# Kernel tuning notes

Measured on AMD Instinct MI355X. Metric: run time of the kernel, lower is better.

The kernel has to match this reference:

```python
import jax, jax.numpy as jnp
import numpy as np

N_NODES = 100000
K_HOPS = 3  # PyG TAGConv default


def _gcn_norm(edge_index, num_nodes):
    # Symmetric normalization WITHOUT self-loops (TAGConv default).
    row, col = edge_index[0], edge_index[1]
    ones = jnp.ones(row.shape[0], dtype=jnp.float32)
    deg = jax.ops.segment_sum(ones, col, num_segments=num_nodes)
    dinv = jnp.where(deg > 0, jax.lax.rsqrt(jnp.maximum(deg, 1.0)), 0.0)
    return dinv[row] * dinv[col]


def _tagconv(x, row, col, norm, W, b, num_nodes):
    # out = Linear(concat_{k=0..K} (D^-1/2 A D^-1/2)^k x)
    xs = [x]
    h = x
    for _ in range(K_HOPS):
        h = jax.ops.segment_sum(norm[:, None] * h[row], col, num_segments=num_nodes)
        xs.append(h)
    return jnp.concatenate(xs, axis=-1) @ W.T + b


def setup_inputs() -> dict:
    key = jax.random.key(0)
    k1, k2, k3, k4, k5 = jax.random.split(key, 5)
    in_c, hid_c, out_c = 128, 128, 128
    n_edges = 1600000
    x = jax.random.normal(k1, (N_NODES, in_c), dtype=jnp.float32)
    edge_index = jax.random.randint(k2, (2, n_edges), 0, N_NODES, dtype=jnp.int64)
    s1 = 1.0 / np.sqrt(in_c * (K_HOPS + 1))
    s2 = 1.0 / np.sqrt(hid_c * (K_HOPS + 1))
    W1 = jax.random.normal(k3, (hid_c, in_c * (K_HOPS + 1)), dtype=jnp.float32) * s1
    b1 = jnp.zeros((hid_c,), dtype=jnp.float32)
    W2 = jax.random.normal(k4, (out_c, hid_c * (K_HOPS + 1)), dtype=jnp.float32) * s2
    b2 = jnp.zeros((out_c,), dtype=jnp.float32)
    return {"x": x, "edge_index": edge_index, "W1": W1, "b1": b1, "W2": W2, "b2": b2}


def reference(x, edge_index, W1, b1, W2, b2):
    row, col = edge_index[0], edge_index[1]
    norm = _gcn_norm(edge_index, N_NODES)  # [E]
    h = jax.nn.relu(_tagconv(x, row, col, norm, W1, b1, N_NODES))
    out = _tagconv(h, row, col, norm, W2, b2, N_NODES)
    return out.reshape(-1)  # original: x.view(n_nodes * out_channels)
```

## Files before the change

kernel.cpp:

```cpp
#include <hip/hip_runtime.h>
#include <hip/hip_fp16.h>

#define FEAT 128
#define SCAN_CHUNK 1024
#define BSH 8
#define BSZ 256
#define NBMAX 400
#define ABLK 4096

typedef _Float16 half_t;
typedef _Float16 half4 __attribute__((ext_vector_type(4)));
typedef _Float16 half8 __attribute__((ext_vector_type(8)));
typedef float float4v __attribute__((ext_vector_type(4)));

__global__ void count_kernel(const int* __restrict__ col, int* __restrict__ deg, int E) {
    int e = blockIdx.x * blockDim.x + threadIdx.x;
    if (e < E) {
        int c = __builtin_nontemporal_load(col + e);
        atomicAdd(&deg[c], 1);
    }
}

__global__ __launch_bounds__(256) void scan_partial_kernel(const int* __restrict__ deg,
                                                           int* __restrict__ partials, int n) {
    __shared__ int sd[256];
    int base = blockIdx.x * SCAN_CHUNK;
    int t = threadIdx.x;
    int s = 0;
#pragma unroll
    for (int j = 0; j < 4; ++j) {
        int i = base + t + j * 256;
        if (i < n) s += deg[i];
    }
    sd[t] = s;
    __syncthreads();
    for (int o = 128; o > 0; o >>= 1) {
        if (t < o) sd[t] += sd[t + o];
        __syncthreads();
    }
    if (t == 0) partials[blockIdx.x] = sd[0];
}

__global__ __launch_bounds__(1024) void scan_top_kernel(int* __restrict__ partials, int nb,
                                                        int* __restrict__ totalp) {
    __shared__ int sd[1024];
    int t = threadIdx.x;
    int v = (t < nb) ? partials[t] : 0;
    sd[t] = v;
    __syncthreads();
    for (int o = 1; o < 1024; o <<= 1) {
        int u = (t >= o) ? sd[t - o] : 0;
        __syncthreads();
        sd[t] += u;
        __syncthreads();
    }
    if (t < nb) partials[t] = sd[t] - v;
    if (t == nb - 1) *totalp = sd[t];
}

__global__ __launch_bounds__(256) void scan_final_kernel(const int* __restrict__ deg,
                                                         const int* __restrict__ partials,
                                                         int* __restrict__ offs,
                                                         float* __restrict__ dinv, int n) {
    __shared__ int sums[256];
    __shared__ int blockoff;
    int base = blockIdx.x * SCAN_CHUNK;
    int t = threadIdx.x;
    int v[4];
    int s = 0;
#pragma unroll
    for (int j = 0; j < 4; ++j) {
        int i = base + 4 * t + j;
        v[j] = (i < n) ? deg[i] : 0;
        s += v[j];
    }
    sums[t] = s;
    if (t == 0) blockoff = partials[blockIdx.x];
    __syncthreads();
    int mine = s;
    for (int o = 1; o < 256; o <<= 1) {
        int u = (t >= o) ? sums[t - o] : 0;
        __syncthreads();
        sums[t] += u;
        __syncthreads();
    }
    int ex = sums[t] - mine + blockoff;
#pragma unroll
    for (int j = 0; j < 4; ++j) {
        int i = base + 4 * t + j;
        if (i < n) {
            offs[i] = ex;
            dinv[i] = (v[j] > 0) ? rsqrtf((float)v[j]) : 0.0f;
        }
        ex += v[j];
    }
}

__global__ void binit_kernel(const int* __restrict__ offs, int* __restrict__ gcur, int NB) {
    int b = blockIdx.x * blockDim.x + threadIdx.x;
    if (b < NB) gcur[b * 16] = offs[b << BSH];
}

__global__ __launch_bounds__(256) void bucketA_kernel(const int* __restrict__ row,
                                                      const int* __restrict__ col,
                                                      int* __restrict__ gcur,
                                                      long long* __restrict__ tmp,
                                                      int E, int NB) {
    __shared__ int hist[NBMAX];
    __shared__ int gbase[NBMAX];
    int t = threadIdx.x;
    int base = blockIdx.x * ABLK;
    for (int i = t; i < NB; i += 256) hist[i] = 0;
    __syncthreads();
    int r[16], c[16];
#pragma unroll
    for (int j = 0; j < 16; ++j) {
        int e = base + j * 256 + t;
        if (e < E) {
            r[j] = __builtin_nontemporal_load(row + e);
            c[j] = __builtin_nontemporal_load(col + e);
            atomicAdd(&hist[c[j] >> BSH], 1);
        } else c[j] = -1;
    }
    __syncthreads();
    for (int b = t; b < NB; b += 256) {
        int cnt = hist[b];
        if (cnt > 0) gbase[b] = atomicAdd(&gcur[b * 16], cnt);
    }
    __syncthreads();
    for (int i = t; i < NB; i += 256) hist[i] = 0;
    __syncthreads();
#pragma unroll
    for (int j = 0; j < 16; ++j) {
        if (c[j] >= 0) {
            int b = c[j] >> BSH;
            int lpos = atomicAdd(&hist[b], 1);
            long long pk = ((long long)(unsigned)c[j] << 32) | (unsigned)r[j];
            tmp[gbase[b] + lpos] = pk;
        }
    }
}

__global__ __launch_bounds__(256) void bfill_kernel(const long long* __restrict__ tmp,
                                                    const int* __restrict__ offs,
                                                    const float* __restrict__ dinv,
                                                    int2* __restrict__ csr, int N) {
    __shared__ int lcur[BSZ];
    int b = blockIdx.x;
    int lo = b << BSH;
    int hi = lo + BSZ;
    if (hi > N) hi = N;
    int t = threadIdx.x;
    if (t < hi - lo) lcur[t] = offs[lo + t];
    __syncthreads();
    int base = offs[lo];
    int end = offs[hi];
    for (int i = base + t; i < end; i += 256) {
        long long pk = __builtin_nontemporal_load(tmp + i);
        int r = (int)(pk & 0xffffffffLL);
        int c = (int)(pk >> 32);
        int pos = atomicAdd(&lcur[c - lo], 1);
        float w = dinv[r] * dinv[c];
        int2 o;
        o.x = r;
        o.y = __float_as_int(w);
        csr[pos] = o;
    }
}

__global__ void f2h3_kernel(const float* __restrict__ a, half_t* __restrict__ ah, int na4,
                            const float* __restrict__ b, half_t* __restrict__ bh, int nb4,
                            const float* __restrict__ c, half_t* __restrict__ ch, int nc4) {
    int i = blockIdx.x * blockDim.x + threadIdx.x;
    const float* src;
    half_t* dst;
    int j = i;
    if (j < na4) { src = a; dst = ah; }
    else if ((j -= na4) < nb4) { src = b; dst = bh; }
    else if ((j -= nb4) < nc4) { src = c; dst = ch; }
    else return;
    float4 v = ((const float4*)src)[j];
    half4 o;
    o.x = (half_t)v.x; o.y = (half_t)v.y; o.z = (half_t)v.z; o.w = (half_t)v.w;
    ((half4*)dst)[j] = o;
}

__global__ __launch_bounds__(256) void prop16_kernel(const half_t* __restrict__ src,
                                                     half_t* __restrict__ dst,
                                                     const int* __restrict__ offs,
                                                     const long long* __restrict__ csr, int N) {
    int v = blockIdx.x * 4 + (threadIdx.x >> 6);
    if (v >= N) return;
    int lane = threadIdx.x & 63;
    int q = lane >> 4;
    int p = lane & 15;
    int s0 = offs[v];
    int s1 = offs[v + 1];
    float acc[8];
#pragma unroll
    for (int j = 0; j < 8; ++j) acc[j] = 0.0f;

    for (int base = s0; base < s1; base += 8) {
        int i0 = base + q;
        int i1 = base + 4 + q;
        long long pk0 = (i0 < s1) ? __builtin_nontemporal_load(csr + i0) : 0LL;
        long long pk1 = (i1 < s1) ? __builtin_nontemporal_load(csr + i1) : 0LL;
        int r0 = (int)(pk0 & 0xffffffffLL);
        int r1 = (int)(pk1 & 0xffffffffLL);
        float w0 = __int_as_float((int)(pk0 >> 32));
        float w1 = __int_as_float((int)(pk1 >> 32));
        half8 va = *(const half8*)(src + (size_t)r0 * FEAT + p * 8);
        half8 vb = *(const half8*)(src + (size_t)r1 * FEAT + p * 8);
#pragma unroll
        for (int j = 0; j < 8; ++j) {
            acc[j] = fmaf(w0, (float)va[j], acc[j]);
            acc[j] = fmaf(w1, (float)vb[j], acc[j]);
        }
    }
#pragma unroll
    for (int j = 0; j < 8; ++j) {
        acc[j] += __shfl_xor(acc[j], 32, 64);
        acc[j] += __shfl_xor(acc[j], 16, 64);
    }
    if (lane < 16) {
        half8 o;
#pragma unroll
        for (int j = 0; j < 8; ++j) o[j] = (half_t)acc[j];
        *(half8*)(dst + (size_t)v * FEAT + p * 8) = o;
    }
}

template <bool RELU, bool HALFOUT>
__global__ __launch_bounds__(256) void gemm16_kernel(const half_t* __restrict__ H0,
                                                     const half_t* __restrict__ H1,
                                                     const half_t* __restrict__ H2,
                                                     const half_t* __restrict__ H3,
                                                     const half_t* __restrict__ W,
                                                     const float* __restrict__ bias,
                                                     half_t* __restrict__ out_h,
                                                     float* __restrict__ out_f, int N) {
    __shared__ half_t ws[128][40];
    const int tid = threadIdx.x;
    const int lane = tid & 63;
    const int wid = tid >> 6;
    const int lr = lane & 15;
    const int lk = lane >> 4;
    const int m = blockIdx.x * 64 + wid * 16 + lr;
    const bool mok = (m < N);

    float4v acc[8];
#pragma unroll
    for (int ct = 0; ct < 8; ++ct) acc[ct] = (float4v)0.0f;

    const half_t* Hs[4] = {H0, H1, H2, H3};
    const int wo = tid >> 1;
    const int wh = tid & 1;

#pragma unroll
    for (int b = 0; b < 4; ++b) {
        const half_t* __restrict__ H = Hs[b];
#pragma unroll
        for (int kt = 0; kt < 128; kt += 32) {
            half8 hfrag = (half8)(half_t)0.0f;
            if (mok) hfrag = *(const half8*)(H + (size_t)m * FEAT + kt + lk * 8);
            const half8* wsrc = (const half8*)(W + (size_t)wo * 512 + b * 128 + kt + wh * 16);
            half8 w0 = wsrc[0];
            half8 w1 = wsrc[1];
            __syncthreads();
            *(half8*)&ws[wo][wh * 16 + 0] = w0;
            *(half8*)&ws[wo][wh * 16 + 8] = w1;
            __syncthreads();
#pragma unroll
            for (int ct = 0; ct < 8; ++ct) {
                half8 wfrag = *(const half8*)&ws[ct * 16 + lr][lk * 8];
                acc[ct] = __builtin_amdgcn_mfma_f32_16x16x32_f16(wfrag, hfrag, acc[ct], 0, 0, 0);
            }
        }
    }

    if (mok) {
#pragma unroll
        for (int ct = 0; ct < 8; ++ct) {
            int o = ct * 16 + lk * 4;
            float4 bv = *(const float4*)(bias + o);
            float r0 = acc[ct][0] + bv.x;
            float r1 = acc[ct][1] + bv.y;
            float r2 = acc[ct][2] + bv.z;
            float r3 = acc[ct][3] + bv.w;
            if (RELU) {
                r0 = fmaxf(r0, 0.0f); r1 = fmaxf(r1, 0.0f);
                r2 = fmaxf(r2, 0.0f); r3 = fmaxf(r3, 0.0f);
            }
            if (HALFOUT) {
                half4 hv;
                hv.x = (half_t)r0; hv.y = (half_t)r1; hv.z = (half_t)r2; hv.w = (half_t)r3;
                *(half4*)(out_h + (size_t)m * FEAT + o) = hv;
            } else {
                float4 fv;
                fv.x = r0; fv.y = r1; fv.z = r2; fv.w = r3;
                *(float4*)(out_f + (size_t)m * FEAT + o) = fv;
            }
        }
    }
}

extern "C" void kernel_launch(void* const* d_in, const int* in_sizes, int n_in,
                              void* d_out, int out_size, void* d_ws, size_t ws_size,
                              hipStream_t stream) {
    const float* x   = (const float*)d_in[0];
    const int*   ei  = (const int*)d_in[1];
    const float* W1  = (const float*)d_in[2];
    const float* b1  = (const float*)d_in[3];
    const float* W2  = (const float*)d_in[4];
    const float* b2  = (const float*)d_in[5];
    float* out = (float*)d_out;

    const int N = in_sizes[0] / FEAT;
    const int E = in_sizes[1] / 2;
    const int* row = ei;
    const int* col = ei + E;
    const int nb = (N + SCAN_CHUNK - 1) / SCAN_CHUNK;
    const int NB = (N + BSZ - 1) / BSZ;

    size_t off = 0;
    auto carve = [&](size_t bytes) -> void* {
        void* p = (char*)d_ws + off;
        off += (bytes + 255) & ~(size_t)255;
        return p;
    };
    int*       deg      = (int*)carve((size_t)N * 4);
    float*     dinv     = (float*)carve((size_t)N * 4);
    int*       offs     = (int*)carve((size_t)(N + 1) * 4);
    int*       partials = (int*)carve((size_t)nb * 4);
    int*       gcur     = (int*)carve((size_t)NB * 16 * 4);
    long long* tmp      = (long long*)carve((size_t)E * 8);
    int2*      csr      = (int2*)carve((size_t)E * 8);
    half_t*    x16      = (half_t*)carve((size_t)N * FEAT * 2);
    half_t*    t1       = (half_t*)carve((size_t)N * FEAT * 2);
    half_t*    t2       = (half_t*)carve((size_t)N * FEAT * 2);
    half_t*    t3       = (half_t*)carve((size_t)N * FEAT * 2);
    half_t*    hbuf     = (half_t*)carve((size_t)N * FEAT * 2);
    half_t*    w1h      = (half_t*)carve((size_t)FEAT * 512 * 2);
    half_t*    w2h      = (half_t*)carve((size_t)FEAT * 512 * 2);

    const int tB = 256;
    const int gE = (E + tB - 1) / tB;
    const int gA = (E + ABLK - 1) / ABLK;
    const int gP = (N + 3) / 4;
    const int gG = (N + 63) / 64;
    const int xt4 = N * FEAT / 4;
    const int wt4 = FEAT * 512 / 4;
    const int cvt_total = xt4 + 2 * wt4;

    hipMemsetAsync(deg, 0, (size_t)N * 4, stream);
    count_kernel<<<gE, tB, 0, stream>>>(col, deg, E);
    scan_partial_kernel<<<nb, 256, 0, stream>>>(deg, partials, N);
    scan_top_kernel<<<1, 1024, 0, stream>>>(partials, nb, offs + N);
    scan_final_kernel<<<nb, 256, 0, stream>>>(deg, partials, offs, dinv, N);
    binit_kernel<<<(NB + tB - 1) / tB, tB, 0, stream>>>(offs, gcur, NB);
    bucketA_kernel<<<gA, 256, 0, stream>>>(row, col, gcur, tmp, E, NB);
    bfill_kernel<<<NB, 256, 0, stream>>>(tmp, offs, dinv, csr, N);

    f2h3_kernel<<<(cvt_total + tB - 1) / tB, tB, 0, stream>>>(x, x16, xt4, W1, w1h, wt4, W2, w2h, wt4);

    const long long* csrll = (const long long*)csr;

    prop16_kernel<<<gP, 256, 0, stream>>>(x16, t1, offs, csrll, N);
    prop16_kernel<<<gP, 256, 0, stream>>>(t1, t2, offs, csrll, N);
    prop16_kernel<<<gP, 256, 0, stream>>>(t2, t3, offs, csrll, N);
    gemm16_kernel<true, true><<<gG, 256, 0, stream>>>(x16, t1, t2, t3, w1h, b1, hbuf, nullptr, N);

    prop16_kernel<<<gP, 256, 0, stream>>>(hbuf, t1, offs, csrll, N);
    prop16_kernel<<<gP, 256, 0, stream>>>(t1, t2, offs, csrll, N);
    prop16_kernel<<<gP, 256, 0, stream>>>(t2, t3, offs, csrll, N);
    gemm16_kernel<false, false><<<gG, 256, 0, stream>>>(hbuf, t1, t2, t3, w2h, b2, nullptr, out, N);
}
```

Before: 593.8 us.

## Bucket edges into fixed-capacity regions and derive degrees per bucket

Drops the global degree-count atomics and the three-kernel prefix scan. Edges are now bucketed straight into fixed-size regions of CAP slots per bucket of 256 nodes. A single-block scan over bucket counts gives the bucket bases. A per-bucket kernel then counts degrees in shared memory to produce offsets and dinv, before the placement pass. This trades one pass of global atomics over all edges for an extra shared-memory read of the bucketed buffer, but it silently assumes no bucket gets more than CAP edges, which holds for uniform random graphs but would overflow on skewed degree distributions.

```diff
diff --git a/kernel.cpp b/kernel.cpp
--- a/kernel.cpp
+++ b/kernel.cpp
@@ -2,103 +2,20 @@
 #include <hip/hip_fp16.h>
 
 #define FEAT 128
-#define SCAN_CHUNK 1024
 #define BSH 8
 #define BSZ 256
 #define NBMAX 400
 #define ABLK 4096
+#define CAP 6144
 
 typedef _Float16 half_t;
 typedef _Float16 half4 __attribute__((ext_vector_type(4)));
 typedef _Float16 half8 __attribute__((ext_vector_type(8)));
 typedef float float4v __attribute__((ext_vector_type(4)));
 
-__global__ void count_kernel(const int* __restrict__ col, int* __restrict__ deg, int E) {
-    int e = blockIdx.x * blockDim.x + threadIdx.x;
-    if (e < E) {
-        int c = __builtin_nontemporal_load(col + e);
-        atomicAdd(&deg[c], 1);
-    }
-}
-
-__global__ __launch_bounds__(256) void scan_partial_kernel(const int* __restrict__ deg,
-                                                           int* __restrict__ partials, int n) {
-    __shared__ int sd[256];
-    int base = blockIdx.x * SCAN_CHUNK;
-    int t = threadIdx.x;
-    int s = 0;
-#pragma unroll
-    for (int j = 0; j < 4; ++j) {
-        int i = base + t + j * 256;
-        if (i < n) s += deg[i];
-    }
-    sd[t] = s;
-    __syncthreads();
-    for (int o = 128; o > 0; o >>= 1) {
-        if (t < o) sd[t] += sd[t + o];
-        __syncthreads();
-    }
-    if (t == 0) partials[blockIdx.x] = sd[0];
-}
-
-__global__ __launch_bounds__(1024) void scan_top_kernel(int* __restrict__ partials, int nb,
-                                                        int* __restrict__ totalp) {
-    __shared__ int sd[1024];
-    int t = threadIdx.x;
-    int v = (t < nb) ? partials[t] : 0;
-    sd[t] = v;
-    __syncthreads();
-    for (int o = 1; o < 1024; o <<= 1) {
-        int u = (t >= o) ? sd[t - o] : 0;
-        __syncthreads();
-        sd[t] += u;
-        __syncthreads();
-    }
-    if (t < nb) partials[t] = sd[t] - v;
-    if (t == nb - 1) *totalp = sd[t];
-}
-
-__global__ __launch_bounds__(256) void scan_final_kernel(const int* __restrict__ deg,
-                                                         const int* __restrict__ partials,
-                                                         int* __restrict__ offs,
-                                                         float* __restrict__ dinv, int n) {
-    __shared__ int sums[256];
-    __shared__ int blockoff;
-    int base = blockIdx.x * SCAN_CHUNK;
-    int t = threadIdx.x;
-    int v[4];
-    int s = 0;
-#pragma unroll
-    for (int j = 0; j < 4; ++j) {
-        int i = base + 4 * t + j;
-        v[j] = (i < n) ? deg[i] : 0;
-        s += v[j];
-    }
-    sums[t] = s;
-    if (t == 0) blockoff = partials[blockIdx.x];
-    __syncthreads();
-    int mine = s;
-    for (int o = 1; o < 256; o <<= 1) {
-        int u = (t >= o) ? sums[t - o] : 0;
-        __syncthreads();
-        sums[t] += u;
-        __syncthreads();
-    }
-    int ex = sums[t] - mine + blockoff;
-#pragma unroll
-    for (int j = 0; j < 4; ++j) {
-        int i = base + 4 * t + j;
-        if (i < n) {
-            offs[i] = ex;
-            dinv[i] = (v[j] > 0) ? rsqrtf((float)v[j]) : 0.0f;
-        }
-        ex += v[j];
-    }
-}
-
-__global__ void binit_kernel(const int* __restrict__ offs, int* __restrict__ gcur, int NB) {
+__global__ void binit_kernel(int* __restrict__ gcur, int NB) {
     int b = blockIdx.x * blockDim.x + threadIdx.x;
-    if (b < NB) gcur[b * 16] = offs[b << BSH];
+    if (b < NB) gcur[b * 16] = b * CAP;
 }
 
 __global__ __launch_bounds__(256) void bucketA_kernel(const int* __restrict__ row,
@@ -141,22 +58,76 @@
     }
 }
 
-__global__ __launch_bounds__(256) void bfill_kernel(const long long* __restrict__ tmp,
-                                                    const int* __restrict__ offs,
-                                                    const float* __restrict__ dinv,
-                                                    int2* __restrict__ csr, int N) {
+__global__ __launch_bounds__(512) void bscan_kernel(const int* __restrict__ gcur,
+                                                    int* __restrict__ bbase,
+                                                    int* __restrict__ offsN, int NB) {
+    __shared__ int sd[512];
+    int t = threadIdx.x;
+    int v = (t < NB) ? (gcur[t * 16] - t * CAP) : 0;
+    sd[t] = v;
+    __syncthreads();
+    for (int o = 1; o < 512; o <<= 1) {
+        int u = (t >= o) ? sd[t - o] : 0;
+        __syncthreads();
+        sd[t] += u;
+        __syncthreads();
+    }
+    if (t < NB) bbase[t] = sd[t] - v;
+    if (t == NB - 1) *offsN = sd[t];
+}
+
+__global__ __launch_bounds__(256) void bdeg_kernel(const long long* __restrict__ tmp,
+                                                   const int* __restrict__ gcur,
+                                                   const int* __restrict__ bbase,
+                                                   int* __restrict__ offs,
+                                                   float* __restrict__ dinv, int N) {
+    __shared__ int ldeg[BSZ];
+    __shared__ int sums[BSZ];
+    int b = blockIdx.x;
+    int lo = b << BSH;
+    int t = threadIdx.x;
+    int cnt = gcur[b * 16] - b * CAP;
+    ldeg[t] = 0;
+    __syncthreads();
+    const long long* reg = tmp + (size_t)b * CAP;
+    for (int i = t; i < cnt; i += 256) {
+        int c = (int)(__builtin_nontemporal_load(reg + i) >> 32);
+        atomicAdd(&ldeg[c - lo], 1);
+    }
+    __syncthreads();
+    int d = ldeg[t];
+    sums[t] = d;
+    __syncthreads();
+    for (int o = 1; o < 256; o <<= 1) {
+        int u = (t >= o) ? sums[t - o] : 0;
+        __syncthreads();
+        sums[t] += u;
+        __syncthreads();
+    }
+    int node = lo + t;
+    if (node < N) {
+        offs[node] = bbase[b] + sums[t] - d;
+        dinv[node] = (d > 0) ? rsqrtf((float)d) : 0.0f;
+    }
+}
+
+__global__ __launch_bounds__(256) void bplace_kernel(const long long* __restrict__ tmp,
+                                                     const int* __restrict__ gcur,
+                                                     const int* __restrict__ offs,
+                                                     const float* __restrict__ dinv,
+                                                     int2* __restrict__ csr, int N) {
     __shared__ int lcur[BSZ];
     int b = blockIdx.x;
     int lo = b << BSH;
     int hi = lo + BSZ;
     if (hi > N) hi = N;
     int t = threadIdx.x;
+    int cnt = gcur[b * 16] - b * CAP;
     if (t < hi - lo) lcur[t] = offs[lo + t];
     __syncthreads();
-    int base = offs[lo];
-    int end = offs[hi];
-    for (int i = base + t; i < end; i += 256) {
-        long long pk = __builtin_nontemporal_load(tmp + i);
+    const long long* reg = tmp + (size_t)b * CAP;
+    for (int i = t; i < cnt; i += 256) {
+        long long pk = __builtin_nontemporal_load(reg + i);
         int r = (int)(pk & 0xffffffffLL);
         int c = (int)(pk >> 32);
         int pos = atomicAdd(&lcur[c - lo], 1);
@@ -319,7 +290,6 @@
     const int E = in_sizes[1] / 2;
     const int* row = ei;
     const int* col = ei + E;
-    const int nb = (N + SCAN_CHUNK - 1) / SCAN_CHUNK;
     const int NB = (N + BSZ - 1) / BSZ;
 
     size_t off = 0;
@@ -328,23 +298,21 @@
         off += (bytes + 255) & ~(size_t)255;
         return p;
     };
-    int*       deg      = (int*)carve((size_t)N * 4);
-    float*     dinv     = (float*)carve((size_t)N * 4);
-    int*       offs     = (int*)carve((size_t)(N + 1) * 4);
-    int*       partials = (int*)carve((size_t)nb * 4);
-    int*       gcur     = (int*)carve((size_t)NB * 16 * 4);
-    long long* tmp      = (long long*)carve((size_t)E * 8);
-    int2*      csr      = (int2*)carve((size_t)E * 8);
-    half_t*    x16      = (half_t*)carve((size_t)N * FEAT * 2);
-    half_t*    t1       = (half_t*)carve((size_t)N * FEAT * 2);
-    half_t*    t2       = (half_t*)carve((size_t)N * FEAT * 2);
-    half_t*    t3       = (half_t*)carve((size_t)N * FEAT * 2);
-    half_t*    hbuf     = (half_t*)carve((size_t)N * FEAT * 2);
-    half_t*    w1h      = (half_t*)carve((size_t)FEAT * 512 * 2);
-    half_t*    w2h      = (half_t*)carve((size_t)FEAT * 512 * 2);
+    float*     dinv = (float*)carve((size_t)N * 4);
+    int*       offs = (int*)carve((size_t)(N + 1) * 4);
+    int*       bbase = (int*)carve((size_t)NB * 4);
+    int*       gcur = (int*)carve((size_t)NB * 16 * 4);
+    long long* tmp  = (long long*)carve((size_t)NB * CAP * 8);
+    int2*      csr  = (int2*)carve((size_t)E * 8);
+    half_t*    x16  = (half_t*)carve((size_t)N * FEAT * 2);
+    half_t*    t1   = (half_t*)carve((size_t)N * FEAT * 2);
+    half_t*    t2   = (half_t*)carve((size_t)N * FEAT * 2);
+    half_t*    t3   = (half_t*)carve((size_t)N * FEAT * 2);
+    half_t*    hbuf = (half_t*)carve((size_t)N * FEAT * 2);
+    half_t*    w1h  = (half_t*)carve((size_t)FEAT * 512 * 2);
+    half_t*    w2h  = (half_t*)carve((size_t)FEAT * 512 * 2);
 
     const int tB = 256;
-    const int gE = (E + tB - 1) / tB;
     const int gA = (E + ABLK - 1) / ABLK;
     const int gP = (N + 3) / 4;
     const int gG = (N + 63) / 64;
@@ -352,14 +320,11 @@
     const int wt4 = FEAT * 512 / 4;
     const int cvt_total = xt4 + 2 * wt4;
 
-    hipMemsetAsync(deg, 0, (size_t)N * 4, stream);
-    count_kernel<<<gE, tB, 0, stream>>>(col, deg, E);
-    scan_partial_kernel<<<nb, 256, 0, stream>>>(deg, partials, N);
-    scan_top_kernel<<<1, 1024, 0, stream>>>(partials, nb, offs + N);
-    scan_final_kernel<<<nb, 256, 0, stream>>>(deg, partials, offs, dinv, N);
-    binit_kernel<<<(NB + tB - 1) / tB, tB, 0, stream>>>(offs, gcur, NB);
+    binit_kernel<<<(NB + tB - 1) / tB, tB, 0, stream>>>(gcur, NB);
     bucketA_kernel<<<gA, 256, 0, stream>>>(row, col, gcur, tmp, E, NB);
-    bfill_kernel<<<NB, 256, 0, stream>>>(tmp, offs, dinv, csr, N);
+    bscan_kernel<<<1, 512, 0, stream>>>(gcur, bbase, offs + N, NB);
+    bdeg_kernel<<<NB, 256, 0, stream>>>(tmp, gcur, bbase, offs, dinv, N);
+    bplace_kernel<<<NB, 256, 0, stream>>>(tmp, gcur, offs, dinv, csr, N);
 
     f2h3_kernel<<<(cvt_total + tB - 1) / tB, tB, 0, stream>>>(x, x16, xt4, W1, w1h, wt4, W2, w2h, wt4);
 
```

Result: faster. 525.8 us (-11.4%).
